# Kernel tuning notes

Hardware: AMD Instinct MI355X
Metric: run time of the kernel (lower is better)

## Reference

```python
import jax, jax.numpy as jnp
import numpy as np

D_MODEL = 256
NHEAD = 8
DK = D_MODEL // NHEAD
EDGE_FEAT_DIM = 7
N_NODES = 2048
N_EDGES = 65536
LN_EPS = 1e-5


def _ln(x, g, b):
    mu = jnp.mean(x, axis=-1, keepdims=True)
    var = jnp.mean(jnp.square(x - mu), axis=-1, keepdims=True)
    return (x - mu) * jax.lax.rsqrt(var + LN_EPS) * g + b


def setup_inputs() -> dict:
    key = jax.random.key(0)
    ks = jax.random.split(key, 16)
    d, h2 = D_MODEL, 2 * D_MODEL
    s = 0.02
    inp = {
        "h": jax.random.normal(ks[0], (N_NODES, d), jnp.float32),
        "edge_attr": jax.random.normal(ks[1], (N_EDGES, EDGE_FEAT_DIM), jnp.float32),
        # weights stored as (in, out): y = x @ W + b (matches torch Linear math)
        "Wq": s * jax.random.normal(ks[2], (d, d), jnp.float32),
        "bq": jnp.zeros((d,), jnp.float32),
        "Wk": s * jax.random.normal(ks[3], (d, d), jnp.float32),
        "bk": jnp.zeros((d,), jnp.float32),
        "Wv": s * jax.random.normal(ks[4], (d, d), jnp.float32),
        "bv": jnp.zeros((d,), jnp.float32),
        "Wo": s * jax.random.normal(ks[5], (d, d), jnp.float32),
        "bo": jnp.zeros((d,), jnp.float32),
        "We": s * jax.random.normal(ks[6], (EDGE_FEAT_DIM, NHEAD), jnp.float32),
        "be": jnp.zeros((NHEAD,), jnp.float32),
        "ln1_g": jnp.ones((d,), jnp.float32),
        "ln1_b": jnp.zeros((d,), jnp.float32),
        "fln_g": jnp.ones((d,), jnp.float32),
        "fln_b": jnp.zeros((d,), jnp.float32),
        "W1": s * jax.random.normal(ks[7], (d, h2), jnp.float32),
        "b1": jnp.zeros((h2,), jnp.float32),
        "W2": s * jax.random.normal(ks[8], (h2, d), jnp.float32),
        "b2": jnp.zeros((d,), jnp.float32),
        "edge_index": jax.random.randint(ks[9], (2, N_EDGES), 0, N_NODES, jnp.int64 if jax.config.jax_enable_x64 else jnp.int32),
    }
    return inp


def reference(h, edge_attr, Wq, bq, Wk, bk, Wv, bv, Wo, bo, We, be,
              ln1_g, ln1_b, fln_g, fln_b, W1, b1, W2, b2, edge_index):
    N = h.shape[0]
    res = h
    # edge bias scattered into dense (N, N, H) tensor
    eb = edge_attr @ We + be                                  # (E, H)
    attn_bias = jnp.zeros((N, N, NHEAD), h.dtype).at[edge_index[0], edge_index[1]].set(eb)
    Q = (h @ Wq + bq).reshape(N, NHEAD, DK)
    K = (h @ Wk + bk).reshape(N, NHEAD, DK)
    V = (h @ Wv + bv).reshape(N, NHEAD, DK)
    scores = jnp.einsum('nhd,mhd->nmh', Q, K) / jnp.sqrt(jnp.float32(DK)) + attn_bias
    attn = jax.nn.softmax(scores, axis=1)                     # softmax over keys m
    out = jnp.einsum('nmh,mhd->nhd', attn, V).reshape(N, D_MODEL)
    out = out @ Wo + bo
    h1 = _ln(res + out, ln1_g, ln1_b)
    ffn = jax.nn.gelu(_ln(h1, fln_g, fln_b) @ W1 + b1, approximate=False) @ W2 + b2
    return h1 + ffn
```

## Files before the change

kernel.cpp:

```cpp
#include <hip/hip_runtime.h>
#include <math.h>

#define NN 2048
#define NE 65536
#define DM 256
#define NH 8
#define DKH 32
#define CAP 128
#define TM2 128
#define SPLIT 4

typedef __attribute__((ext_vector_type(8))) short bf16x8;
typedef __attribute__((ext_vector_type(4))) float f32x4;

#define WAVE_LDS_SYNC() __asm__ volatile("s_waitcnt lgkmcnt(0)" ::: "memory")

__device__ __forceinline__ unsigned short f2b(float f) {
    unsigned u = __float_as_uint(f);
    unsigned r = (u + 0x7FFFu + ((u >> 16) & 1u)) >> 16;
    return (unsigned short)r;
}
__device__ __forceinline__ float b2f(unsigned short s) {
    return __uint_as_float(((unsigned)s) << 16);
}
__device__ __forceinline__ unsigned pk2(float a, float b) {
    unsigned ua = __float_as_uint(a) + 0x8000u;
    unsigned ub = __float_as_uint(b) + 0x8000u;
    return (ua >> 16) | (ub & 0xFFFF0000u);
}

__global__ __launch_bounds__(256) void prep_all_kernel(
    const float* __restrict__ Wq, const float* __restrict__ Wk,
    const float* __restrict__ Wv, const float* __restrict__ Wo,
    const float* __restrict__ W1, const float* __restrict__ W2,
    const float* __restrict__ ea, const float* __restrict__ We,
    const float* __restrict__ be, const int* __restrict__ ei,
    unsigned short* __restrict__ Wqkvt, unsigned short* __restrict__ Wot,
    unsigned short* __restrict__ W1t, unsigned short* __restrict__ W2t,
    float* __restrict__ eb, int* __restrict__ cnt, int* __restrict__ lst)
{
    int b = blockIdx.x;
    if (b < 2048) {
        int i = b * 256 + threadIdx.x;
        if (i < 196608) {
            int n = i >> 8, k = i & 255;
            const float* W = (n < 256) ? Wq : (n < 512) ? Wk : Wv;
            Wqkvt[i] = f2b(W[k * 256 + (n & 255)]);
        } else if (i < 262144) {
            int j = i - 196608;
            int n = j >> 8, k = j & 255;
            Wot[j] = f2b(Wo[k * 256 + n]);
        } else if (i < 393216) {
            int j = i - 262144;
            int n = j >> 8, k = j & 255;
            W1t[j] = f2b(W1[(size_t)k * 512 + n]);
        } else {
            int j = i - 393216;
            int n = j >> 9, k = j & 511;
            W2t[j] = f2b(W2[(size_t)k * 256 + n]);
        }
    } else {
        int e = (b - 2048) * 256 + threadIdx.x;
        float acc[NH];
#pragma unroll
        for (int hh = 0; hh < NH; ++hh) acc[hh] = be[hh];
#pragma unroll
        for (int f = 0; f < 7; ++f) {
            float x = ea[e * 7 + f];
#pragma unroll
            for (int hh = 0; hh < NH; ++hh) acc[hh] = fmaf(x, We[f * NH + hh], acc[hh]);
        }
#pragma unroll
        for (int hh = 0; hh < NH; ++hh)
            eb[e * NH + hh] = acc[hh] * 1.44269504088896f;
        int s = ei[e];
        int p = atomicAdd(&cnt[s], 1);
        if (p < CAP) lst[s * CAP + p] = e;
    }
}

__global__ __launch_bounds__(128) void rowprep_kernel(
    const int* __restrict__ ei, const int* __restrict__ cnt,
    const int* __restrict__ lst, int* __restrict__ sortedDest,
    int* __restrict__ sortedE, int* __restrict__ rowOff)
{
    __shared__ int ds[CAP], es[CAP];
    __shared__ int bc[16], off[17];
    int n = blockIdx.x, t = threadIdx.x;
    int c = cnt[n]; if (c > CAP) c = CAP;
    if (t < 16) bc[t] = 0;
    int e = -1, d = -1;
    if (t < c) { e = lst[n * CAP + t]; d = ei[NE + e]; }
    ds[t] = d; es[t] = e;
    __syncthreads();
    bool win = (t < c);
    if (win) {
        for (int j = 0; j < c; ++j)
            if (ds[j] == d && es[j] > e) { win = false; break; }
    }
    int bkt = (d >= 0) ? (d >> 7) : 0;
    int pos = -1;
    if (win) pos = atomicAdd(&bc[bkt], 1);
    __syncthreads();
    if (t == 0) {
        int s = 0;
        for (int i = 0; i < 16; ++i) { off[i] = s; s += bc[i]; }
        off[16] = s;
    }
    __syncthreads();
    if (win) {
        int p = off[bkt] + pos;
        sortedDest[n * CAP + p] = d;
        sortedE[n * CAP + p] = e;
    }
    if (t < 17) rowOff[n * 17 + t] = off[t];
}

template <int EPI, int MT, int AF32>
__global__ __launch_bounds__(MT * 4) void gemm_bf16(
    const void* __restrict__ Av, const unsigned short* __restrict__ Bt,
    const float* __restrict__ bias0, const float* __restrict__ bias1,
    const float* __restrict__ bias2, const float* __restrict__ resid,
    void* __restrict__ out0, void* __restrict__ out1, void* __restrict__ out2,
    int M, int N, int K)
{
    __shared__ __align__(16) unsigned short As[MT][136];
    __shared__ __align__(16) unsigned short Bs[64][136];
    int tid = threadIdx.x;
    int wv = tid >> 6, l = tid & 63, l15 = l & 15, quad = l >> 4;
    int m0 = blockIdx.y * MT, n0 = blockIdx.x * 64;

    f32x4 acc[4];
#pragma unroll
    for (int i = 0; i < 4; ++i) acc[i] = (f32x4){0.f, 0.f, 0.f, 0.f};

    for (int k0 = 0; k0 < K; k0 += 128) {
        if (MT == 64) {
            int row = tid >> 2, cb = (tid & 3) * 32;
            if (AF32) {
                const float* ap = (const float*)Av + (size_t)(m0 + row) * K + k0 + cb;
#pragma unroll
                for (int i = 0; i < 4; ++i) {
                    float4 f0 = *(const float4*)(ap + i * 8);
                    float4 f1 = *(const float4*)(ap + i * 8 + 4);
                    uint4 pk = { pk2(f0.x, f0.y), pk2(f0.z, f0.w),
                                 pk2(f1.x, f1.y), pk2(f1.z, f1.w) };
                    *(uint4*)&As[row][cb + i * 8] = pk;
                }
            } else {
                const unsigned short* ap =
                    (const unsigned short*)Av + (size_t)(m0 + row) * K + k0 + cb;
#pragma unroll
                for (int i = 0; i < 4; ++i)
                    *(uint4*)&As[row][cb + i * 8] = *(const uint4*)(ap + i * 8);
            }
            const unsigned short* bp = Bt + (size_t)(n0 + row) * K + k0 + cb;
#pragma unroll
            for (int i = 0; i < 4; ++i)
                *(uint4*)&Bs[row][cb + i * 8] = *(const uint4*)(bp + i * 8);
        } else {
            int rowa = tid >> 2, cba = (tid & 3) * 32;
            const unsigned short* ap =
                (const unsigned short*)Av + (size_t)(m0 + rowa) * K + k0 + cba;
#pragma unroll
            for (int i = 0; i < 4; ++i)
                *(uint4*)&As[rowa][cba + i * 8] = *(const uint4*)(ap + i * 8);
            int rowb = tid >> 1, cbb = (tid & 1) * 64;
            const unsigned short* bp = Bt + (size_t)(n0 + rowb) * K + k0 + cbb;
#pragma unroll
            for (int i = 0; i < 8; ++i)
                *(uint4*)&Bs[rowb][cbb + i * 8] = *(const uint4*)(bp + i * 8);
        }
        __syncthreads();
#pragma unroll
        for (int ks = 0; ks < 4; ++ks) {
            bf16x8 a = *(const bf16x8*)&As[wv * 16 + l15][ks * 32 + quad * 8];
#pragma unroll
            for (int nt = 0; nt < 4; ++nt) {
                bf16x8 b = *(const bf16x8*)&Bs[nt * 16 + l15][ks * 32 + quad * 8];
                acc[nt] = __builtin_amdgcn_mfma_f32_16x16x32_bf16(a, b, acc[nt], 0, 0, 0);
            }
        }
        __syncthreads();
    }

#pragma unroll
    for (int nt = 0; nt < 4; ++nt) {
        int colb = n0 + nt * 16;
        if (EPI == 2 && colb >= 512) {
            int n = colb + l15 - 512;
            float bv = bias2[n];
            uint2 pk = { pk2(acc[nt][0] + bv, acc[nt][1] + bv),
                         pk2(acc[nt][2] + bv, acc[nt][3] + bv) };
            *(uint2*)((unsigned short*)out2 + (size_t)n * NN + m0 + wv * 16 + quad * 4) = pk;
            continue;
        }
#pragma unroll
        for (int r = 0; r < 4; ++r) {
            int row = m0 + wv * 16 + quad * 4 + r;
            int col = colb + l15;
            float v = acc[nt][r];
            if (EPI == 0) {
                v += bias0[col];
                if (resid) v += resid[(size_t)row * N + col];
                ((float*)out0)[(size_t)row * N + col] = v;
            } else if (EPI == 1) {
                v += bias0[col];
                v = 0.5f * v * (1.0f + erff(v * 0.70710678118654752f));
                ((unsigned short*)out0)[(size_t)row * N + col] = f2b(v);
            } else {
                if (col < 256) {
                    v = (v + bias0[col]) * 0.2550348592f;
                    ((unsigned short*)out0)[(size_t)row * 256 + col] = f2b(v);
                } else {
                    v += bias1[col - 256];
                    ((unsigned short*)out1)[(size_t)row * 256 + col - 256] = f2b(v);
                }
            }
        }
    }
}

__global__ __launch_bounds__(256) void attn_mfma(
    const unsigned short* __restrict__ Qb, const unsigned short* __restrict__ Kb,
    const unsigned short* __restrict__ Vt, const float* __restrict__ eb,
    const int* __restrict__ sortedDest, const int* __restrict__ sortedE,
    const int* __restrict__ rowOff,
    float* __restrict__ accD, float* __restrict__ lD)
{
    __shared__ __align__(16) unsigned short Ks[TM2][40];
    __shared__ __align__(16) unsigned short Vs[32][TM2 + 8];
    __shared__ __align__(16) unsigned short Pn[4][16][TM2 + 16];
    int h = blockIdx.y, tid = threadIdx.x;
    int wv = tid >> 6, l = tid & 63, l15 = l & 15, quad = l >> 4;
    int n0 = blockIdx.x * 64 + wv * 16;
    int mz = blockIdx.z;

    bf16x8 aq = *(const bf16x8*)(Qb + (size_t)(n0 + l15) * DM + h * 32 + quad * 8);

    f32x4 oacc[2];
    oacc[0] = (f32x4){0.f, 0.f, 0.f, 0.f};
    oacc[1] = (f32x4){0.f, 0.f, 0.f, 0.f};
    float lacc = 0.f;
    float dreg = 0.f;
    const unsigned short* Vth = Vt + (size_t)h * 32 * NN;

    int r16 = l >> 2, sub = l & 3;
    int frow = n0 + r16;

    for (int t = 0; t < NN / (TM2 * SPLIT); ++t) {
        int m0 = (mz * (NN / SPLIT)) + t * TM2;
        int ti = m0 >> 7;
        {
            int r = tid >> 1, kc = (tid & 1) * 16;
            const unsigned short* ks = Kb + (size_t)(m0 + r) * DM + h * 32 + kc;
            *(uint4*)&Ks[r][kc]     = *(const uint4*)(ks);
            *(uint4*)&Ks[r][kc + 8] = *(const uint4*)(ks + 8);
            int d = tid >> 3, mc = (tid & 7) * 16;
            const unsigned short* vs = Vth + (size_t)d * NN + m0 + mc;
            *(uint4*)&Vs[d][mc]     = *(const uint4*)(vs);
            *(uint4*)&Vs[d][mc + 8] = *(const uint4*)(vs + 8);
        }
        __syncthreads();
#pragma unroll
        for (int mt = 0; mt < TM2 / 16; ++mt) {
            bf16x8 ak = *(const bf16x8*)&Ks[mt * 16 + l15][quad * 8];
            f32x4 s = __builtin_amdgcn_mfma_f32_16x16x32_bf16(
                ak, aq, (f32x4){0.f, 0.f, 0.f, 0.f}, 0, 0, 0);
            float p0 = __builtin_amdgcn_exp2f(s[0]);
            float p1 = __builtin_amdgcn_exp2f(s[1]);
            float p2 = __builtin_amdgcn_exp2f(s[2]);
            float p3 = __builtin_amdgcn_exp2f(s[3]);
            lacc += (p0 + p1) + (p2 + p3);
            *(uint2*)&Pn[wv][l15][mt * 16 + quad * 4] =
                (uint2){pk2(p0, p1), pk2(p2, p3)};
        }
        WAVE_LDS_SYNC();
        {
            int o0 = rowOff[frow * 17 + ti];
            int o1 = rowOff[frow * 17 + ti + 1];
            for (int idx = o0 + sub; idx < o1; idx += 4) {
                int d = sortedDest[frow * CAP + idx] - m0;
                int e = sortedE[frow * CAP + idx];
                float expb = __builtin_amdgcn_exp2f(eb[e * NH + h]);
                float pold = b2f(Pn[wv][r16][d]);
                Pn[wv][r16][d] = f2b(pold * expb);
                dreg += pold * (expb - 1.0f);
            }
        }
        WAVE_LDS_SYNC();
#pragma unroll
        for (int kc = 0; kc < TM2 / 32; ++kc) {
            bf16x8 ap = *(const bf16x8*)&Pn[wv][l15][kc * 32 + quad * 8];
#pragma unroll
            for (int nt = 0; nt < 2; ++nt) {
                bf16x8 bv = *(const bf16x8*)&Vs[nt * 16 + l15][kc * 32 + quad * 8];
                oacc[nt] = __builtin_amdgcn_mfma_f32_16x16x32_bf16(ap, bv, oacc[nt], 0, 0, 0);
            }
        }
        __syncthreads();
    }

    lacc += __shfl_xor(lacc, 16);
    lacc += __shfl_xor(lacc, 32);
    dreg += __shfl_xor(dreg, 1);
    dreg += __shfl_xor(dreg, 2);
    float dtot = __shfl(dreg, l15 * 4);
    float* lDp = lD + (size_t)mz * NN * NH;
    if (l < 16)
        lDp[(size_t)(n0 + l) * NH + h] = lacc + dtot;
    float* aDp = accD + (size_t)mz * NN * DM;
#pragma unroll
    for (int nt = 0; nt < 2; ++nt)
#pragma unroll
        for (int r = 0; r < 4; ++r)
            aDp[(size_t)(n0 + quad * 4 + r) * DM + h * 32 + nt * 16 + l15] = oacc[nt][r];
}

__global__ __launch_bounds__(256) void tail_fused_kernel(
    const float* __restrict__ accD, const float* __restrict__ lD,
    const unsigned short* __restrict__ Wot, const float* __restrict__ bo,
    const float* __restrict__ h, const float* __restrict__ ln1g,
    const float* __restrict__ ln1b, const float* __restrict__ flng,
    const float* __restrict__ flnb,
    const unsigned short* __restrict__ W1t, const float* __restrict__ fb1,
    const unsigned short* __restrict__ W2t, const float* __restrict__ fb2,
    float* __restrict__ out)
{
    __shared__ float linv[16][8];
    __shared__ __align__(16) unsigned short As[16][264];
    __shared__ __align__(16) unsigned short Wfs[512][40];
    __shared__ float Tt[16][264];
    __shared__ __align__(16) unsigned short X2s[16][264];
    __shared__ __align__(16) unsigned short F1s[16][520];
    int tid = threadIdx.x, m0 = blockIdx.x * 16;
    int wv = tid >> 6, l = tid & 63, l15 = l & 15, quad = l >> 4;

    if (tid < 128) {
        int r = tid >> 3, hh = tid & 7;
        float ls = 0.f;
#pragma unroll
        for (int s = 0; s < SPLIT; ++s)
            ls += lD[(size_t)s * NN * NH + (size_t)(m0 + r) * NH + hh];
        linv[r][hh] = 1.0f / ls;
    }
    __syncthreads();
#pragma unroll
    for (int ch = 0; ch < 16; ++ch) {
        float o = 0.f;
#pragma unroll
        for (int s = 0; s < SPLIT; ++s)
            o += accD[(size_t)s * NN * DM + (size_t)(m0 + ch) * DM + tid];
        As[ch][tid] = f2b(o * linv[ch][tid >> 5]);
    }
    __syncthreads();

    f32x4 acc[4];
#pragma unroll
    for (int i = 0; i < 4; ++i) acc[i] = (f32x4){0.f, 0.f, 0.f, 0.f};

    for (int k0 = 0; k0 < 256; k0 += 32) {
#pragma unroll
        for (int ps = 0; ps < 4; ++ps) {
            int row = ps * 64 + (tid >> 2), kk = (tid & 3) * 8;
            *(uint4*)&Wfs[row][kk] = *(const uint4*)(Wot + (size_t)row * 256 + k0 + kk);
        }
        __syncthreads();
        bf16x8 a = *(const bf16x8*)&As[l15][k0 + quad * 8];
#pragma unroll
        for (int nt = 0; nt < 4; ++nt) {
            bf16x8 b = *(const bf16x8*)&Wfs[wv * 64 + nt * 16 + l15][quad * 8];
            acc[nt] = __builtin_amdgcn_mfma_f32_16x16x32_bf16(a, b, acc[nt], 0, 0, 0);
        }
        __syncthreads();
    }

#pragma unroll
    for (int nt = 0; nt < 4; ++nt)
#pragma unroll
        for (int r = 0; r < 4; ++r) {
            int row = quad * 4 + r, col = wv * 64 + nt * 16 + l15;
            Tt[row][col] = acc[nt][r] + bo[col] + h[(size_t)(m0 + row) * DM + col];
        }
    __syncthreads();

    int rr = tid >> 4, l16 = tid & 15;
    float x[16];
#pragma unroll
    for (int j = 0; j < 16; ++j) x[j] = Tt[rr][l16 + 16 * j];
    float mu = 0.f;
#pragma unroll
    for (int j = 0; j < 16; ++j) mu += x[j];
#pragma unroll
    for (int off = 1; off < 16; off <<= 1) mu += __shfl_xor(mu, off);
    mu *= (1.0f / 256.0f);
    float var = 0.f;
#pragma unroll
    for (int j = 0; j < 16; ++j) { float d = x[j] - mu; var += d * d; }
#pragma unroll
    for (int off = 1; off < 16; off <<= 1) var += __shfl_xor(var, off);
    float rs = rsqrtf(var * (1.0f / 256.0f) + 1e-5f);
    float y[16]; float mu2 = 0.f;
#pragma unroll
    for (int j = 0; j < 16; ++j) {
        int c = l16 + 16 * j;
        y[j] = (x[j] - mu) * rs * ln1g[c] + ln1b[c];
        mu2 += y[j];
    }
#pragma unroll
    for (int off = 1; off < 16; off <<= 1) mu2 += __shfl_xor(mu2, off);
    mu2 *= (1.0f / 256.0f);
    float var2 = 0.f;
#pragma unroll
    for (int j = 0; j < 16; ++j) { float d = y[j] - mu2; var2 += d * d; }
#pragma unroll
    for (int off = 1; off < 16; off <<= 1) var2 += __shfl_xor(var2, off);
    float rs2 = rsqrtf(var2 * (1.0f / 256.0f) + 1e-5f);
#pragma unroll
    for (int j = 0; j < 16; ++j) {
        int c = l16 + 16 * j;
        Tt[rr][c] = y[j];
        X2s[rr][c] = f2b((y[j] - mu2) * rs2 * flng[c] + flnb[c]);
    }
    __syncthreads();

    f32x4 acc1[8];
#pragma unroll
    for (int i = 0; i < 8; ++i) acc1[i] = (f32x4){0.f, 0.f, 0.f, 0.f};

    for (int k0 = 0; k0 < 256; k0 += 32) {
#pragma unroll
        for (int ps = 0; ps < 8; ++ps) {
            int row = ps * 64 + (tid >> 2), kk = (tid & 3) * 8;
            *(uint4*)&Wfs[row][kk] = *(const uint4*)(W1t + (size_t)row * 256 + k0 + kk);
        }
        __syncthreads();
        bf16x8 a = *(const bf16x8*)&X2s[l15][k0 + quad * 8];
#pragma unroll
        for (int nt = 0; nt < 8; ++nt) {
            bf16x8 b = *(const bf16x8*)&Wfs[wv * 128 + nt * 16 + l15][quad * 8];
            acc1[nt] = __builtin_amdgcn_mfma_f32_16x16x32_bf16(a, b, acc1[nt], 0, 0, 0);
        }
        __syncthreads();
    }
#pragma unroll
    for (int nt = 0; nt < 8; ++nt)
#pragma unroll
        for (int r = 0; r < 4; ++r) {
            int row = quad * 4 + r, col = wv * 128 + nt * 16 + l15;
            float v = acc1[nt][r] + fb1[col];
            v = 0.5f * v * (1.0f + erff(v * 0.70710678118654752f));
            F1s[row][col] = f2b(v);
        }

    f32x4 acc2[4];
#pragma unroll
    for (int i = 0; i < 4; ++i) acc2[i] = (f32x4){0.f, 0.f, 0.f, 0.f};

    for (int k0 = 0; k0 < 512; k0 += 32) {
#pragma unroll
        for (int ps = 0; ps < 4; ++ps) {
            int row = ps * 64 + (tid >> 2), kk = (tid & 3) * 8;
            *(uint4*)&Wfs[row][kk] = *(const uint4*)(W2t + (size_t)row * 512 + k0 + kk);
        }
        __syncthreads();
        bf16x8 a = *(const bf16x8*)&F1s[l15][k0 + quad * 8];
#pragma unroll
        for (int nt = 0; nt < 4; ++nt) {
            bf16x8 b = *(const bf16x8*)&Wfs[wv * 64 + nt * 16 + l15][quad * 8];
            acc2[nt] = __builtin_amdgcn_mfma_f32_16x16x32_bf16(a, b, acc2[nt], 0, 0, 0);
        }
        __syncthreads();
    }
#pragma unroll
    for (int nt = 0; nt < 4; ++nt)
#pragma unroll
        for (int r = 0; r < 4; ++r) {
            int row = quad * 4 + r, col = wv * 64 + nt * 16 + l15;
            out[(size_t)(m0 + row) * DM + col] = acc2[nt][r] + fb2[col] + Tt[row][col];
        }
}

extern "C" void kernel_launch(void* const* d_in, const int* in_sizes, int n_in,
                              void* d_out, int out_size, void* d_ws, size_t ws_size,
                              hipStream_t stream)
{
    const float* h    = (const float*)d_in[0];
    const float* ea   = (const float*)d_in[1];
    const float* Wq   = (const float*)d_in[2];
    const float* bq   = (const float*)d_in[3];
    const float* Wk   = (const float*)d_in[4];
    const float* bk   = (const float*)d_in[5];
    const float* Wv   = (const float*)d_in[6];
    const float* bv   = (const float*)d_in[7];
    const float* Wo   = (const float*)d_in[8];
    const float* bo   = (const float*)d_in[9];
    const float* We   = (const float*)d_in[10];
    const float* be   = (const float*)d_in[11];
    const float* ln1g = (const float*)d_in[12];
    const float* ln1b = (const float*)d_in[13];
    const float* flng = (const float*)d_in[14];
    const float* flnb = (const float*)d_in[15];
    const float* W1   = (const float*)d_in[16];
    const float* b1   = (const float*)d_in[17];
    const float* W2   = (const float*)d_in[18];
    const float* b2   = (const float*)d_in[19];
    const int*   ei   = (const int*)d_in[20];
    float* out = (float*)d_out;

    char* p = (char*)d_ws;
    float* eb   = (float*)p;           p += (size_t)NE * NH * 4;
    int*   cnt  = (int*)p;             p += (size_t)NN * 4;
    int*   lst  = (int*)p;             p += (size_t)NN * CAP * 4;
    int*   sD   = (int*)p;             p += (size_t)NN * CAP * 4;
    int*   sE   = (int*)p;             p += (size_t)NN * CAP * 4;
    int*   rOff = (int*)p;             p += (size_t)NN * 17 * 4;
    unsigned short* Wqkvt = (unsigned short*)p; p += (size_t)768 * 256 * 2;
    unsigned short* Wot   = (unsigned short*)p; p += (size_t)256 * 256 * 2;
    unsigned short* W1t   = (unsigned short*)p; p += (size_t)512 * 256 * 2;
    unsigned short* W2t   = (unsigned short*)p; p += (size_t)256 * 512 * 2;
    unsigned short* Qb    = (unsigned short*)p; p += (size_t)NN * DM * 2;
    unsigned short* Kb    = (unsigned short*)p; p += (size_t)NN * DM * 2;
    unsigned short* Vt    = (unsigned short*)p; p += (size_t)NN * DM * 2;
    float* accD = (float*)p;           p += (size_t)SPLIT * NN * DM * 4;
    float* lD   = (float*)p;           p += (size_t)SPLIT * NN * NH * 4;

    hipMemsetAsync(cnt, 0, (size_t)NN * 4, stream);
    prep_all_kernel<<<2048 + NE / 256, 256, 0, stream>>>(
        Wq, Wk, Wv, Wo, W1, W2, ea, We, be, ei,
        Wqkvt, Wot, W1t, W2t, eb, cnt, lst);
    rowprep_kernel<<<NN, 128, 0, stream>>>(ei, cnt, lst, sD, sE, rOff);

    gemm_bf16<2, 64, 1><<<dim3(768 / 64, NN / 64), 256, 0, stream>>>(
        h, Wqkvt, bq, bk, bv, nullptr, Qb, Kb, Vt, NN, 768, 256);

    attn_mfma<<<dim3(NN / 64, NH, SPLIT), 256, 0, stream>>>(
        Qb, Kb, Vt, eb, sD, sE, rOff, accD, lD);

    tail_fused_kernel<<<NN / 16, 256, 0, stream>>>(
        accD, lD, Wot, bo, h, ln1g, ln1b, flng, flnb,
        W1t, b1, W2t, b2, out);
}
```

Baseline: 172.8 us.

## Read tail-kernel weights directly from global memory and double block threads

The fused tail kernel drops its shared-memory weight staging buffer and the per-k-step barriers. Each wave now loads its MFMA B operands straight from global (L2-cached) bf16 weights. The block grows from 256 to 512 threads, so each wave owns fewer output columns, and the layer norm runs on half the threads. This targets barrier stalls and the staging copies, and adds occupancy by freeing about 40KB of LDS per block. The trade-off is uncoalesced-ish 16-byte global loads with no cross-wave reuse, which shifts pressure onto L2.

```diff
diff --git a/kernel.cpp b/kernel.cpp
--- a/kernel.cpp
+++ b/kernel.cpp
@@ -317,7 +317,7 @@
             aDp[(size_t)(n0 + quad * 4 + r) * DM + h * 32 + nt * 16 + l15] = oacc[nt][r];
 }
 
-__global__ __launch_bounds__(256) void tail_fused_kernel(
+__global__ __launch_bounds__(512) void tail_fused_kernel(
     const float* __restrict__ accD, const float* __restrict__ lD,
     const unsigned short* __restrict__ Wot, const float* __restrict__ bo,
     const float* __restrict__ h, const float* __restrict__ ln1g,
@@ -329,7 +329,6 @@
 {
     __shared__ float linv[16][8];
     __shared__ __align__(16) unsigned short As[16][264];
-    __shared__ __align__(16) unsigned short Wfs[512][40];
     __shared__ float Tt[16][264];
     __shared__ __align__(16) unsigned short X2s[16][264];
     __shared__ __align__(16) unsigned short F1s[16][520];
@@ -345,138 +344,126 @@
         linv[r][hh] = 1.0f / ls;
     }
     __syncthreads();
-#pragma unroll
-    for (int ch = 0; ch < 16; ++ch) {
-        float o = 0.f;
-#pragma unroll
-        for (int s = 0; s < SPLIT; ++s)
-            o += accD[(size_t)s * NN * DM + (size_t)(m0 + ch) * DM + tid];
-        As[ch][tid] = f2b(o * linv[ch][tid >> 5]);
-    }
-    __syncthreads();
-
-    f32x4 acc[4];
-#pragma unroll
-    for (int i = 0; i < 4; ++i) acc[i] = (f32x4){0.f, 0.f, 0.f, 0.f};
-
+    {
+        int col = tid & 255, rh = tid >> 8;
+#pragma unroll
+        for (int ch = 0; ch < 8; ++ch) {
+            int row = ch * 2 + rh;
+            float o = 0.f;
+#pragma unroll
+            for (int s = 0; s < SPLIT; ++s)
+                o += accD[(size_t)s * NN * DM + (size_t)(m0 + row) * DM + col];
+            As[row][col] = f2b(o * linv[row][col >> 5]);
+        }
+    }
+    __syncthreads();
+
+    f32x4 acc[2];
+    acc[0] = (f32x4){0.f, 0.f, 0.f, 0.f};
+    acc[1] = (f32x4){0.f, 0.f, 0.f, 0.f};
+#pragma unroll
     for (int k0 = 0; k0 < 256; k0 += 32) {
-#pragma unroll
-        for (int ps = 0; ps < 4; ++ps) {
-            int row = ps * 64 + (tid >> 2), kk = (tid & 3) * 8;
-            *(uint4*)&Wfs[row][kk] = *(const uint4*)(Wot + (size_t)row * 256 + k0 + kk);
-        }
-        __syncthreads();
         bf16x8 a = *(const bf16x8*)&As[l15][k0 + quad * 8];
 #pragma unroll
+        for (int nt = 0; nt < 2; ++nt) {
+            int row = wv * 32 + nt * 16 + l15;
+            bf16x8 b = *(const bf16x8*)(Wot + (size_t)row * 256 + k0 + quad * 8);
+            acc[nt] = __builtin_amdgcn_mfma_f32_16x16x32_bf16(a, b, acc[nt], 0, 0, 0);
+        }
+    }
+#pragma unroll
+    for (int nt = 0; nt < 2; ++nt)
+#pragma unroll
+        for (int r = 0; r < 4; ++r) {
+            int row = quad * 4 + r, col = wv * 32 + nt * 16 + l15;
+            Tt[row][col] = acc[nt][r] + bo[col] + h[(size_t)(m0 + row) * DM + col];
+        }
+    __syncthreads();
+
+    if (tid < 256) {
+        int rr = tid >> 4, l16 = tid & 15;
+        float x[16];
+#pragma unroll
+        for (int j = 0; j < 16; ++j) x[j] = Tt[rr][l16 + 16 * j];
+        float mu = 0.f;
+#pragma unroll
+        for (int j = 0; j < 16; ++j) mu += x[j];
+#pragma unroll
+        for (int off = 1; off < 16; off <<= 1) mu += __shfl_xor(mu, off);
+        mu *= (1.0f / 256.0f);
+        float var = 0.f;
+#pragma unroll
+        for (int j = 0; j < 16; ++j) { float d = x[j] - mu; var += d * d; }
+#pragma unroll
+        for (int off = 1; off < 16; off <<= 1) var += __shfl_xor(var, off);
+        float rs = rsqrtf(var * (1.0f / 256.0f) + 1e-5f);
+        float y[16]; float mu2 = 0.f;
+#pragma unroll
+        for (int j = 0; j < 16; ++j) {
+            int c = l16 + 16 * j;
+            y[j] = (x[j] - mu) * rs * ln1g[c] + ln1b[c];
+            mu2 += y[j];
+        }
+#pragma unroll
+        for (int off = 1; off < 16; off <<= 1) mu2 += __shfl_xor(mu2, off);
+        mu2 *= (1.0f / 256.0f);
+        float var2 = 0.f;
+#pragma unroll
+        for (int j = 0; j < 16; ++j) { float d = y[j] - mu2; var2 += d * d; }
+#pragma unroll
+        for (int off = 1; off < 16; off <<= 1) var2 += __shfl_xor(var2, off);
+        float rs2 = rsqrtf(var2 * (1.0f / 256.0f) + 1e-5f);
+#pragma unroll
+        for (int j = 0; j < 16; ++j) {
+            int c = l16 + 16 * j;
+            Tt[rr][c] = y[j];
+            X2s[rr][c] = f2b((y[j] - mu2) * rs2 * flng[c] + flnb[c]);
+        }
+    }
+    __syncthreads();
+
+    f32x4 acc1[4];
+#pragma unroll
+    for (int i = 0; i < 4; ++i) acc1[i] = (f32x4){0.f, 0.f, 0.f, 0.f};
+#pragma unroll
+    for (int k0 = 0; k0 < 256; k0 += 32) {
+        bf16x8 a = *(const bf16x8*)&X2s[l15][k0 + quad * 8];
+#pragma unroll
         for (int nt = 0; nt < 4; ++nt) {
-            bf16x8 b = *(const bf16x8*)&Wfs[wv * 64 + nt * 16 + l15][quad * 8];
-            acc[nt] = __builtin_amdgcn_mfma_f32_16x16x32_bf16(a, b, acc[nt], 0, 0, 0);
-        }
-        __syncthreads();
-    }
-
+            int row = wv * 64 + nt * 16 + l15;
+            bf16x8 b = *(const bf16x8*)(W1t + (size_t)row * 256 + k0 + quad * 8);
+            acc1[nt] = __builtin_amdgcn_mfma_f32_16x16x32_bf16(a, b, acc1[nt], 0, 0, 0);
+        }
+    }
 #pragma unroll
     for (int nt = 0; nt < 4; ++nt)
 #pragma unroll
         for (int r = 0; r < 4; ++r) {
             int row = quad * 4 + r, col = wv * 64 + nt * 16 + l15;
-            Tt[row][col] = acc[nt][r] + bo[col] + h[(size_t)(m0 + row) * DM + col];
-        }
-    __syncthreads();
-
-    int rr = tid >> 4, l16 = tid & 15;
-    float x[16];
-#pragma unroll
-    for (int j = 0; j < 16; ++j) x[j] = Tt[rr][l16 + 16 * j];
-    float mu = 0.f;
-#pragma unroll
-    for (int j = 0; j < 16; ++j) mu += x[j];
-#pragma unroll
-    for (int off = 1; off < 16; off <<= 1) mu += __shfl_xor(mu, off);
-    mu *= (1.0f / 256.0f);
-    float var = 0.f;
-#pragma unroll
-    for (int j = 0; j < 16; ++j) { float d = x[j] - mu; var += d * d; }
-#pragma unroll
-    for (int off = 1; off < 16; off <<= 1) var += __shfl_xor(var, off);
-    float rs = rsqrtf(var * (1.0f / 256.0f) + 1e-5f);
-    float y[16]; float mu2 = 0.f;
-#pragma unroll
-    for (int j = 0; j < 16; ++j) {
-        int c = l16 + 16 * j;
-        y[j] = (x[j] - mu) * rs * ln1g[c] + ln1b[c];
-        mu2 += y[j];
-    }
-#pragma unroll
-    for (int off = 1; off < 16; off <<= 1) mu2 += __shfl_xor(mu2, off);
-    mu2 *= (1.0f / 256.0f);
-    float var2 = 0.f;
-#pragma unroll
-    for (int j = 0; j < 16; ++j) { float d = y[j] - mu2; var2 += d * d; }
-#pragma unroll
-    for (int off = 1; off < 16; off <<= 1) var2 += __shfl_xor(var2, off);
-    float rs2 = rsqrtf(var2 * (1.0f / 256.0f) + 1e-5f);
-#pragma unroll
-    for (int j = 0; j < 16; ++j) {
-        int c = l16 + 16 * j;
-        Tt[rr][c] = y[j];
-        X2s[rr][c] = f2b((y[j] - mu2) * rs2 * flng[c] + flnb[c]);
-    }
-    __syncthreads();
-
-    f32x4 acc1[8];
-#pragma unroll
-    for (int i = 0; i < 8; ++i) acc1[i] = (f32x4){0.f, 0.f, 0.f, 0.f};
-
-    for (int k0 = 0; k0 < 256; k0 += 32) {
-#pragma unroll
-        for (int ps = 0; ps < 8; ++ps) {
-            int row = ps * 64 + (tid >> 2), kk = (tid & 3) * 8;
-            *(uint4*)&Wfs[row][kk] = *(const uint4*)(W1t + (size_t)row * 256 + k0 + kk);
-        }
-        __syncthreads();
-        bf16x8 a = *(const bf16x8*)&X2s[l15][k0 + quad * 8];
-#pragma unroll
-        for (int nt = 0; nt < 8; ++nt) {
-            bf16x8 b = *(const bf16x8*)&Wfs[wv * 128 + nt * 16 + l15][quad * 8];
-            acc1[nt] = __builtin_amdgcn_mfma_f32_16x16x32_bf16(a, b, acc1[nt], 0, 0, 0);
-        }
-        __syncthreads();
-    }
-#pragma unroll
-    for (int nt = 0; nt < 8; ++nt)
-#pragma unroll
-        for (int r = 0; r < 4; ++r) {
-            int row = quad * 4 + r, col = wv * 128 + nt * 16 + l15;
             float v = acc1[nt][r] + fb1[col];
             v = 0.5f * v * (1.0f + erff(v * 0.70710678118654752f));
             F1s[row][col] = f2b(v);
         }
-
-    f32x4 acc2[4];
-#pragma unroll
-    for (int i = 0; i < 4; ++i) acc2[i] = (f32x4){0.f, 0.f, 0.f, 0.f};
-
+    __syncthreads();
+
+    f32x4 acc2[2];
+    acc2[0] = (f32x4){0.f, 0.f, 0.f, 0.f};
+    acc2[1] = (f32x4){0.f, 0.f, 0.f, 0.f};
+#pragma unroll
     for (int k0 = 0; k0 < 512; k0 += 32) {
-#pragma unroll
-        for (int ps = 0; ps < 4; ++ps) {
-            int row = ps * 64 + (tid >> 2), kk = (tid & 3) * 8;
-            *(uint4*)&Wfs[row][kk] = *(const uint4*)(W2t + (size_t)row * 512 + k0 + kk);
-        }
-        __syncthreads();
         bf16x8 a = *(const bf16x8*)&F1s[l15][k0 + quad * 8];
 #pragma unroll
-        for (int nt = 0; nt < 4; ++nt) {
-            bf16x8 b = *(const bf16x8*)&Wfs[wv * 64 + nt * 16 + l15][quad * 8];
+        for (int nt = 0; nt < 2; ++nt) {
+            int row = wv * 32 + nt * 16 + l15;
+            bf16x8 b = *(const bf16x8*)(W2t + (size_t)row * 512 + k0 + quad * 8);
             acc2[nt] = __builtin_amdgcn_mfma_f32_16x16x32_bf16(a, b, acc2[nt], 0, 0, 0);
         }
-        __syncthreads();
-    }
-#pragma unroll
-    for (int nt = 0; nt < 4; ++nt)
+    }
+#pragma unroll
+    for (int nt = 0; nt < 2; ++nt)
 #pragma unroll
         for (int r = 0; r < 4; ++r) {
-            int row = quad * 4 + r, col = wv * 64 + nt * 16 + l15;
+            int row = quad * 4 + r, col = wv * 32 + nt * 16 + l15;
             out[(size_t)(m0 + row) * DM + col] = acc2[nt][r] + fb2[col] + Tt[row][col];
         }
 }
@@ -537,7 +524,7 @@
     attn_mfma<<<dim3(NN / 64, NH, SPLIT), 256, 0, stream>>>(
         Qb, Kb, Vt, eb, sD, sE, rOff, accD, lD);
 
-    tail_fused_kernel<<<NN / 16, 256, 0, stream>>>(
+    tail_fused_kernel<<<NN / 16, 512, 0, stream>>>(
         accD, lD, Wot, bo, h, ln1g, ln1b, flng, flnb,
         W1t, b1, W2t, b2, out);
 }
```

New measurement: 173.8 us. About the same (+0.6%).
